# Optimization experiments

Hardware: AMD Instinct MI355X
Metric: run time of the kernel (lower is better)

The kernel has to match this reference:

```python
import jax, jax.numpy as jnp
import numpy as np

B, T, DE, DR, H = 8192, 8, 512, 1024, 1024


def setup_inputs() -> dict:
    key = jax.random.key(0)
    ks = jax.random.split(key, 8)
    std = 1.0 / np.sqrt(H)
    u = lambda k, shape: jax.random.uniform(k, shape, jnp.float32, -std, std)
    return {
        "entity": jax.random.normal(ks[0], (B, T, DE), jnp.float32),
        "relation": jax.random.normal(ks[1], (B, T, DR), jnp.float32),
        "We": u(ks[2], (H, DE)),
        "be": u(ks[3], (H,)),
        "Wr": u(ks[4], (H, DR)),
        "br": u(ks[5], (H,)),
        "Wh": u(ks[6], (H, H)),
        "bh": u(ks[7], (H,)),
    }


def reference(entity, relation, We, be, Wr, br, Wh, bh):
    # entity: [B, T, DE], relation: [B, T, DR]
    # Precompute time-parallel input projections (linear, math-equivalent to per-step).
    g = (jnp.einsum("btd,hd->bth", entity, We) + be
         + jnp.einsum("btd,hd->bth", relation, Wr) + br)  # [B, T, H]

    def step(h, gt):
        h = jax.nn.relu(gt + h @ Wh.T + bh)  # RNNCell_rel: relu(e2h(e)+r2h(r)+h2h(h))
        return h, h

    h0 = jnp.zeros((entity.shape[0], Wh.shape[0]), entity.dtype)
    hn, outs = jax.lax.scan(step, h0, jnp.transpose(g, (1, 0, 2)))  # outs: [T, B, H]
    output = jnp.transpose(outs, (1, 0, 2))  # [B, T, H] (batch-first)
    need = hn.T  # faithful to hidden[0].transpose(0,1): [H, B]
    return output, need
```

## Files before the change

kernel.cpp:

```cpp
#include <hip/hip_runtime.h>
#include <hip/hip_bf16.h>

#define BB 8192
#define TT 8
#define DEe 512
#define DRr 1024
#define HH 1024
#define KTOT 2560

typedef __attribute__((ext_vector_type(8))) __bf16 bf16x8;
typedef __attribute__((ext_vector_type(4))) __bf16 bf16x4;
typedef __attribute__((ext_vector_type(4))) float f32x4;

__device__ __forceinline__ void gld_lds16(const __bf16* g, __bf16* l) {
    __builtin_amdgcn_global_load_lds(
        (const __attribute__((address_space(1))) void*)g,
        (__attribute__((address_space(3))) void*)l, 16, 0, 0);
}

__global__ void pack_a(const float* __restrict__ ent, const float* __restrict__ rel,
                       __bf16* __restrict__ buf, int t) {
    const int b = blockIdx.y;
    const int sec = blockIdx.x;
    const int i = threadIdx.x;
    float4 v; size_t dst;
    if (sec == 0) {
        v = *(const float4*)(ent + ((size_t)b * TT + t) * DEe + i * 4);
        dst = (size_t)b * KTOT + i * 4;
    } else {
        int d = (sec - 1) * 512 + i * 4;
        v = *(const float4*)(rel + ((size_t)b * TT + t) * DRr + d);
        dst = (size_t)b * KTOT + DEe + d;
    }
    bf16x4 o = {(__bf16)v.x, (__bf16)v.y, (__bf16)v.z, (__bf16)v.w};
    *(bf16x4*)(buf + dst) = o;
}

__global__ void pack_b(const float* __restrict__ We, const float* __restrict__ Wr,
                       const float* __restrict__ Wh, __bf16* __restrict__ Bw) {
    const int n = blockIdx.y;
    const int sec = blockIdx.x;
    const int i = threadIdx.x;
    float4 v; size_t dst;
    if (sec == 0) {
        v = *(const float4*)(We + (size_t)n * DEe + i * 4);
        dst = (size_t)n * KTOT + i * 4;
    } else if (sec <= 2) {
        int d = (sec - 1) * 512 + i * 4;
        v = *(const float4*)(Wr + (size_t)n * DRr + d);
        dst = (size_t)n * KTOT + DEe + d;
    } else {
        int d = (sec - 3) * 512 + i * 4;
        v = *(const float4*)(Wh + (size_t)n * HH + d);
        dst = (size_t)n * KTOT + 1536 + d;
    }
    bf16x4 o = {(__bf16)v.x, (__bf16)v.y, (__bf16)v.z, (__bf16)v.w};
    *(bf16x4*)(Bw + dst) = o;
}

__global__ __launch_bounds__(256) void gemm_step(
    const __bf16* __restrict__ A, const __bf16* __restrict__ Bw,
    const float* __restrict__ be, const float* __restrict__ br,
    const float* __restrict__ bh,
    float* __restrict__ out, __bf16* __restrict__ Anext,
    float* __restrict__ need, int K, int t) {
    __shared__ __bf16 sA[128 * 32];
    __shared__ __bf16 sB[128 * 32];
    __shared__ float sBias[128];

    const int tid  = threadIdx.x;
    const int lane = tid & 63;
    const int w    = tid >> 6;
    const int tileM = blockIdx.y * 128;
    const int tileN = blockIdx.x * 128;

    if (tid < 128) {
        int n = tileN + tid;
        sBias[tid] = be[n] + br[n] + bh[n];
    }

    const int r0 = (w * 2 + 0) * 16 + (lane >> 2);
    const int r1 = (w * 2 + 1) * 16 + (lane >> 2);
    const int cc = (lane & 3) * 8;
    const __bf16* gA0 = A + (size_t)(tileM + r0) * KTOT + cc;
    const __bf16* gA1 = A + (size_t)(tileM + r1) * KTOT + cc;
    const __bf16* gB0 = Bw + (size_t)(tileN + r0) * KTOT + cc;
    const __bf16* gB1 = Bw + (size_t)(tileN + r1) * KTOT + cc;
    __bf16* lA0 = sA + (w * 2 + 0) * 512;
    __bf16* lA1 = sA + (w * 2 + 1) * 512;
    __bf16* lB0 = sB + (w * 2 + 0) * 512;
    __bf16* lB1 = sB + (w * 2 + 1) * 512;

    const int wm = (w >> 1) * 64, wn = (w & 1) * 64;
    const int fm = lane & 15, fq = lane >> 4;

    f32x4 acc[4][4];
#pragma unroll
    for (int i = 0; i < 4; i++)
#pragma unroll
        for (int j = 0; j < 4; j++) acc[i][j] = {0.f, 0.f, 0.f, 0.f};

    for (int k0 = 0; k0 < K; k0 += 32) {
        gld_lds16(gA0 + k0, lA0);
        gld_lds16(gA1 + k0, lA1);
        gld_lds16(gB0 + k0, lB0);
        gld_lds16(gB1 + k0, lB1);
        __syncthreads();
        bf16x8 af[4], bf[4];
#pragma unroll
        for (int mf = 0; mf < 4; mf++)
            af[mf] = *(const bf16x8*)&sA[(wm + mf * 16 + fm) * 32 + fq * 8];
#pragma unroll
        for (int nf = 0; nf < 4; nf++)
            bf[nf] = *(const bf16x8*)&sB[(wn + nf * 16 + fm) * 32 + fq * 8];
#pragma unroll
        for (int mf = 0; mf < 4; mf++)
#pragma unroll
            for (int nf = 0; nf < 4; nf++)
                acc[mf][nf] = __builtin_amdgcn_mfma_f32_16x16x32_bf16(
                    af[mf], bf[nf], acc[mf][nf], 0, 0, 0);
        __syncthreads();
    }

#pragma unroll
    for (int mf = 0; mf < 4; mf++) {
#pragma unroll
        for (int nf = 0; nf < 4; nf++) {
            f32x4 v = acc[mf][nf];
            const int nl = wn + nf * 16 + fm;
            const int n  = tileN + nl;
            const int m0 = tileM + wm + mf * 16 + fq * 4;
            const float bias = sBias[nl];
            float hv[4];
#pragma unroll
            for (int r = 0; r < 4; r++) {
                float x = v[r] + bias;
                hv[r] = x > 0.f ? x : 0.f;
                out[(size_t)(m0 + r) * (TT * HH) + (size_t)t * HH + n] = hv[r];
                if (Anext)
                    Anext[(size_t)(m0 + r) * KTOT + 1536 + n] = (__bf16)hv[r];
            }
            if (need) {
                f32x4 nv = {hv[0], hv[1], hv[2], hv[3]};
                *(f32x4*)&need[(size_t)n * BB + m0] = nv;
            }
        }
    }
}

extern "C" void kernel_launch(void* const* d_in, const int* in_sizes, int n_in,
                              void* d_out, int out_size, void* d_ws, size_t ws_size,
                              hipStream_t stream) {
    const float* ent = (const float*)d_in[0];
    const float* rel = (const float*)d_in[1];
    const float* We  = (const float*)d_in[2];
    const float* be  = (const float*)d_in[3];
    const float* Wr  = (const float*)d_in[4];
    const float* br  = (const float*)d_in[5];
    const float* Wh  = (const float*)d_in[6];
    const float* bh  = (const float*)d_in[7];

    float* out  = (float*)d_out;
    float* need = out + (size_t)BB * TT * HH;

    char* ws = (char*)d_ws;
    __bf16* buf0 = (__bf16*)ws;
    __bf16* buf1 = (__bf16*)(ws + (size_t)BB * KTOT * 2);
    __bf16* Bw   = (__bf16*)(ws + (size_t)2 * BB * KTOT * 2);
    __bf16* bufs[2] = {buf0, buf1};

    pack_b<<<dim3(5, 1024), 128, 0, stream>>>(We, Wr, Wh, Bw);
    for (int t = 0; t < TT; t++) {
        pack_a<<<dim3(3, BB), 128, 0, stream>>>(ent, rel, bufs[t & 1], t);
        gemm_step<<<dim3(8, 64), 256, 0, stream>>>(
            bufs[t & 1], Bw, be, br, bh, out,
            (t < 7) ? bufs[(t + 1) & 1] : nullptr,
            (t == 7) ? need : nullptr,
            (t == 0) ? 1536 : KTOT, t);
    }
}
```

Baseline: 1.153 ms.

## Hoist input projections into one batched GEMM, recurrence GEMMs only on Wh

Computes the entity/relation projections for all timesteps in a single large bf16 GEMM that writes pre-activations (plus biases) into the output buffer. Each recurrent step then only multiplies the hidden state by Wh, adds the stored pre-activation, and applies relu. This removes the per-step packing kernels and runs the input work as one big, well-occupied GEMM. It also adds a block-index swizzle for L2 locality. In exchange, each step's epilogue must read back the fp32 output tensor.

After: 1.286 ms. 11.5% more time.

```diff
diff --git a/kernel.cpp b/kernel.cpp
--- a/kernel.cpp
+++ b/kernel.cpp
@@ -6,7 +6,8 @@
 #define DEe 512
 #define DRr 1024
 #define HH 1024
-#define KTOT 2560
+#define KG 1536
+#define MG 65536
 
 typedef __attribute__((ext_vector_type(8))) __bf16 bf16x8;
 typedef __attribute__((ext_vector_type(4))) __bf16 bf16x4;
@@ -18,52 +19,49 @@
         (__attribute__((address_space(3))) void*)l, 16, 0, 0);
 }
 
-__global__ void pack_a(const float* __restrict__ ent, const float* __restrict__ rel,
-                       __bf16* __restrict__ buf, int t) {
-    const int b = blockIdx.y;
-    const int sec = blockIdx.x;
-    const int i = threadIdx.x;
-    float4 v; size_t dst;
-    if (sec == 0) {
-        v = *(const float4*)(ent + ((size_t)b * TT + t) * DEe + i * 4);
-        dst = (size_t)b * KTOT + i * 4;
-    } else {
-        int d = (sec - 1) * 512 + i * 4;
-        v = *(const float4*)(rel + ((size_t)b * TT + t) * DRr + d);
-        dst = (size_t)b * KTOT + DEe + d;
-    }
-    bf16x4 o = {(__bf16)v.x, (__bf16)v.y, (__bf16)v.z, (__bf16)v.w};
-    *(bf16x4*)(buf + dst) = o;
-}
-
-__global__ void pack_b(const float* __restrict__ We, const float* __restrict__ Wr,
-                       const float* __restrict__ Wh, __bf16* __restrict__ Bw) {
+__global__ void pack_ga(const float* __restrict__ ent, const float* __restrict__ rel,
+                        __bf16* __restrict__ ga) {
+    const int total = MG * (KG / 4);
+    const int stride = gridDim.x * blockDim.x;
+    for (int g = blockIdx.x * blockDim.x + threadIdx.x; g < total; g += stride) {
+        int m = g / 384;
+        int c4 = g - m * 384;
+        float4 v;
+        if (c4 < 128) v = ((const float4*)ent)[(size_t)m * 128 + c4];
+        else          v = ((const float4*)rel)[(size_t)m * 256 + (c4 - 128)];
+        bf16x4 o = {(__bf16)v.x, (__bf16)v.y, (__bf16)v.z, (__bf16)v.w};
+        *(bf16x4*)(ga + (size_t)m * KG + c4 * 4) = o;
+    }
+}
+
+__global__ void pack_bw(const float* __restrict__ We, const float* __restrict__ Wr,
+                        const float* __restrict__ Wh,
+                        __bf16* __restrict__ BW, __bf16* __restrict__ WhP) {
     const int n = blockIdx.y;
     const int sec = blockIdx.x;
     const int i = threadIdx.x;
-    float4 v; size_t dst;
+    float4 v; __bf16* dst;
     if (sec == 0) {
         v = *(const float4*)(We + (size_t)n * DEe + i * 4);
-        dst = (size_t)n * KTOT + i * 4;
+        dst = BW + (size_t)n * KG + i * 4;
     } else if (sec <= 2) {
         int d = (sec - 1) * 512 + i * 4;
         v = *(const float4*)(Wr + (size_t)n * DRr + d);
-        dst = (size_t)n * KTOT + DEe + d;
+        dst = BW + (size_t)n * KG + DEe + d;
     } else {
         int d = (sec - 3) * 512 + i * 4;
         v = *(const float4*)(Wh + (size_t)n * HH + d);
-        dst = (size_t)n * KTOT + 1536 + d;
+        dst = WhP + (size_t)n * HH + d;
     }
     bf16x4 o = {(__bf16)v.x, (__bf16)v.y, (__bf16)v.z, (__bf16)v.w};
-    *(bf16x4*)(Bw + dst) = o;
-}
-
-__global__ __launch_bounds__(256) void gemm_step(
+    *(bf16x4*)dst = o;
+}
+
+__global__ __launch_bounds__(256) void gemm_g(
     const __bf16* __restrict__ A, const __bf16* __restrict__ Bw,
     const float* __restrict__ be, const float* __restrict__ br,
     const float* __restrict__ bh,
-    float* __restrict__ out, __bf16* __restrict__ Anext,
-    float* __restrict__ need, int K, int t) {
+    float* __restrict__ out, __bf16* __restrict__ h0) {
     __shared__ __bf16 sA[128 * 32];
     __shared__ __bf16 sB[128 * 32];
     __shared__ float sBias[128];
@@ -71,8 +69,10 @@
     const int tid  = threadIdx.x;
     const int lane = tid & 63;
     const int w    = tid >> 6;
-    const int tileM = blockIdx.y * 128;
-    const int tileN = blockIdx.x * 128;
+    const int bid  = blockIdx.y * 8 + blockIdx.x;
+    const int swz  = (bid & 7) * 512 + (bid >> 3);
+    const int tileN = (swz & 7) * 128;
+    const int tileM = (swz >> 3) * 128;
 
     if (tid < 128) {
         int n = tileN + tid;
@@ -82,10 +82,10 @@
     const int r0 = (w * 2 + 0) * 16 + (lane >> 2);
     const int r1 = (w * 2 + 1) * 16 + (lane >> 2);
     const int cc = (lane & 3) * 8;
-    const __bf16* gA0 = A + (size_t)(tileM + r0) * KTOT + cc;
-    const __bf16* gA1 = A + (size_t)(tileM + r1) * KTOT + cc;
-    const __bf16* gB0 = Bw + (size_t)(tileN + r0) * KTOT + cc;
-    const __bf16* gB1 = Bw + (size_t)(tileN + r1) * KTOT + cc;
+    const __bf16* gA0 = A + (size_t)(tileM + r0) * KG + cc;
+    const __bf16* gA1 = A + (size_t)(tileM + r1) * KG + cc;
+    const __bf16* gB0 = Bw + (size_t)(tileN + r0) * KG + cc;
+    const __bf16* gB1 = Bw + (size_t)(tileN + r1) * KG + cc;
     __bf16* lA0 = sA + (w * 2 + 0) * 512;
     __bf16* lA1 = sA + (w * 2 + 1) * 512;
     __bf16* lB0 = sB + (w * 2 + 0) * 512;
@@ -100,7 +100,7 @@
 #pragma unroll
         for (int j = 0; j < 4; j++) acc[i][j] = {0.f, 0.f, 0.f, 0.f};
 
-    for (int k0 = 0; k0 < K; k0 += 32) {
+    for (int k0 = 0; k0 < KG; k0 += 32) {
         gld_lds16(gA0 + k0, lA0);
         gld_lds16(gA1 + k0, lA1);
         gld_lds16(gB0 + k0, lB0);
@@ -131,14 +131,97 @@
             const int n  = tileN + nl;
             const int m0 = tileM + wm + mf * 16 + fq * 4;
             const float bias = sBias[nl];
-            float hv[4];
+            const bool t0row = ((m0 & 7) == 0);
 #pragma unroll
             for (int r = 0; r < 4; r++) {
                 float x = v[r] + bias;
+                size_t m = (size_t)(m0 + r);
+                if (t0row && r == 0) {
+                    float hv = x > 0.f ? x : 0.f;
+                    out[m * HH + n] = hv;
+                    h0[(m >> 3) * HH + n] = (__bf16)hv;
+                } else {
+                    out[m * HH + n] = x;
+                }
+            }
+        }
+    }
+}
+
+__global__ __launch_bounds__(256) void gemm_step(
+    const __bf16* __restrict__ A, const __bf16* __restrict__ Bw,
+    float* __restrict__ out, __bf16* __restrict__ hn,
+    float* __restrict__ need, int t) {
+    __shared__ __bf16 sA[128 * 32];
+    __shared__ __bf16 sB[128 * 32];
+
+    const int tid  = threadIdx.x;
+    const int lane = tid & 63;
+    const int w    = tid >> 6;
+    const int bid  = blockIdx.y * 8 + blockIdx.x;
+    const int swz  = (bid & 7) * 64 + (bid >> 3);
+    const int tileN = (swz & 7) * 128;
+    const int tileM = (swz >> 3) * 128;
+
+    const int r0 = (w * 2 + 0) * 16 + (lane >> 2);
+    const int r1 = (w * 2 + 1) * 16 + (lane >> 2);
+    const int cc = (lane & 3) * 8;
+    const __bf16* gA0 = A + (size_t)(tileM + r0) * HH + cc;
+    const __bf16* gA1 = A + (size_t)(tileM + r1) * HH + cc;
+    const __bf16* gB0 = Bw + (size_t)(tileN + r0) * HH + cc;
+    const __bf16* gB1 = Bw + (size_t)(tileN + r1) * HH + cc;
+    __bf16* lA0 = sA + (w * 2 + 0) * 512;
+    __bf16* lA1 = sA + (w * 2 + 1) * 512;
+    __bf16* lB0 = sB + (w * 2 + 0) * 512;
+    __bf16* lB1 = sB + (w * 2 + 1) * 512;
+
+    const int wm = (w >> 1) * 64, wn = (w & 1) * 64;
+    const int fm = lane & 15, fq = lane >> 4;
+
+    f32x4 acc[4][4];
+#pragma unroll
+    for (int i = 0; i < 4; i++)
+#pragma unroll
+        for (int j = 0; j < 4; j++) acc[i][j] = {0.f, 0.f, 0.f, 0.f};
+
+    for (int k0 = 0; k0 < HH; k0 += 32) {
+        gld_lds16(gA0 + k0, lA0);
+        gld_lds16(gA1 + k0, lA1);
+        gld_lds16(gB0 + k0, lB0);
+        gld_lds16(gB1 + k0, lB1);
+        __syncthreads();
+        bf16x8 af[4], bf[4];
+#pragma unroll
+        for (int mf = 0; mf < 4; mf++)
+            af[mf] = *(const bf16x8*)&sA[(wm + mf * 16 + fm) * 32 + fq * 8];
+#pragma unroll
+        for (int nf = 0; nf < 4; nf++)
+            bf[nf] = *(const bf16x8*)&sB[(wn + nf * 16 + fm) * 32 + fq * 8];
+#pragma unroll
+        for (int mf = 0; mf < 4; mf++)
+#pragma unroll
+            for (int nf = 0; nf < 4; nf++)
+                acc[mf][nf] = __builtin_amdgcn_mfma_f32_16x16x32_bf16(
+                    af[mf], bf[nf], acc[mf][nf], 0, 0, 0);
+        __syncthreads();
+    }
+
+#pragma unroll
+    for (int mf = 0; mf < 4; mf++) {
+#pragma unroll
+        for (int nf = 0; nf < 4; nf++) {
+            f32x4 v = acc[mf][nf];
+            const int nl = wn + nf * 16 + fm;
+            const int n  = tileN + nl;
+            const int m0 = tileM + wm + mf * 16 + fq * 4;
+            float hv[4];
+#pragma unroll
+            for (int r = 0; r < 4; r++) {
+                size_t addr = ((size_t)(m0 + r) * TT + t) * HH + n;
+                float x = v[r] + out[addr];
                 hv[r] = x > 0.f ? x : 0.f;
-                out[(size_t)(m0 + r) * (TT * HH) + (size_t)t * HH + n] = hv[r];
-                if (Anext)
-                    Anext[(size_t)(m0 + r) * KTOT + 1536 + n] = (__bf16)hv[r];
+                out[addr] = hv[r];
+                if (hn) hn[(size_t)(m0 + r) * HH + n] = (__bf16)hv[r];
             }
             if (need) {
                 f32x4 nv = {hv[0], hv[1], hv[2], hv[3]};
@@ -164,18 +247,20 @@
     float* need = out + (size_t)BB * TT * HH;
 
     char* ws = (char*)d_ws;
-    __bf16* buf0 = (__bf16*)ws;
-    __bf16* buf1 = (__bf16*)(ws + (size_t)BB * KTOT * 2);
-    __bf16* Bw   = (__bf16*)(ws + (size_t)2 * BB * KTOT * 2);
-    __bf16* bufs[2] = {buf0, buf1};
-
-    pack_b<<<dim3(5, 1024), 128, 0, stream>>>(We, Wr, Wh, Bw);
-    for (int t = 0; t < TT; t++) {
-        pack_a<<<dim3(3, BB), 128, 0, stream>>>(ent, rel, bufs[t & 1], t);
+    __bf16* GA  = (__bf16*)ws;
+    __bf16* BW  = (__bf16*)(ws + (size_t)MG * KG * 2);
+    __bf16* WhP = (__bf16*)(ws + (size_t)MG * KG * 2 + (size_t)HH * KG * 2);
+    __bf16* hA  = (__bf16*)((char*)WhP + (size_t)HH * HH * 2);
+    __bf16* hB  = (__bf16*)((char*)hA + (size_t)BB * HH * 2);
+    __bf16* hbuf[2] = {hA, hB};
+
+    pack_bw<<<dim3(5, 1024), 128, 0, stream>>>(We, Wr, Wh, BW, WhP);
+    pack_ga<<<dim3(2048), 256, 0, stream>>>(ent, rel, GA);
+    gemm_g<<<dim3(8, 512), 256, 0, stream>>>(GA, BW, be, br, bh, out, hA);
+    for (int t = 1; t < TT; t++) {
         gemm_step<<<dim3(8, 64), 256, 0, stream>>>(
-            bufs[t & 1], Bw, be, br, bh, out,
-            (t < 7) ? bufs[(t + 1) & 1] : nullptr,
-            (t == 7) ? need : nullptr,
-            (t == 0) ? 1536 : KTOT, t);
-    }
-}
+            hbuf[(t - 1) & 1], WhP, out,
+            (t < 7) ? hbuf[t & 1] : nullptr,
+            (t == 7) ? need : nullptr, t);
+    }
+}
```
